# Kernel optimization log

Hardware: AMD Instinct MI355X
Metric: run time of the kernel (lower is better)

## Reference

```python
import jax, jax.numpy as jnp
import numpy as np

P, N, GRID, C, S, STEPS, N_ADJ = 128, 512, 112, 64, 128, 3, 4
HW = GRID * GRID
IN_DIM = C + 2


def _ring_adjacency():
    # prepare_gcn_component builds a ring graph: each vertex connected to
    # n_adj nearest neighbors along the polygon, row-normalized.
    offs = np.concatenate([np.arange(1, N_ADJ // 2 + 1), -np.arange(1, N_ADJ // 2 + 1)])
    A = np.zeros((N, N), np.float32)
    idx = np.arange(N)
    for o in offs:
        A[idx, (idx + o) % N] = 1.0
    A /= A.sum(1, keepdims=True)
    return jnp.asarray(A)


def setup_inputs() -> dict:
    key = jax.random.key(0)
    ks = jax.random.split(key, 10)
    std = 0.01  # matches m.weight.data.normal_(0.0, 0.01)
    return {
        "feature": jax.random.normal(ks[0], (P, HW, C), jnp.float32),
        "init_polys": jax.random.uniform(ks[1], (P, N, 2), jnp.float32),
        "adj": _ring_adjacency(),
        "W1s": jax.random.normal(ks[2], (STEPS, IN_DIM, S), jnp.float32) * std,
        "W1n": jax.random.normal(ks[3], (STEPS, IN_DIM, S), jnp.float32) * std,
        "b1": jnp.zeros((STEPS, S), jnp.float32),
        "W2s": jax.random.normal(ks[4], (STEPS, S, S), jnp.float32) * std,
        "W2n": jax.random.normal(ks[5], (STEPS, S, S), jnp.float32) * std,
        "b2": jnp.zeros((STEPS, S), jnp.float32),
        "Wfc": jax.random.normal(ks[6], (STEPS, S, 2), jnp.float32) * std,
        "bfc": jnp.zeros((STEPS, 2), jnp.float32),
    }


def _gather(feat, ids):
    # feat: [P, HW, C], ids: [P, N] int -> [P, N, C]
    return jnp.take_along_axis(feat, ids[:, :, None], axis=1)


def _nearest_sample(feature, poly):
    # step-0 `sampling` path: gather at floor(coord*grid) flat indices
    X0 = jnp.clip(jnp.floor(poly[..., 0] * GRID), 0, GRID - 1)
    Y0 = jnp.clip(jnp.floor(poly[..., 1] * GRID), 0, GRID - 1)
    ids = (X0 + Y0 * GRID).astype(jnp.int32)
    return _gather(feature, ids)


def _interpolated_sum(feature, poly):
    Xs = poly[..., 0] * GRID
    Ys = poly[..., 1] * GRID
    X0 = jnp.floor(Xs); X1 = X0 + 1.0
    Y0 = jnp.floor(Ys); Y1 = Y0 + 1.0
    w00 = (X1 - Xs) * (Y1 - Ys)
    w01 = (X1 - Xs) * (Ys - Y0)
    w10 = (Xs - X0) * (Y1 - Ys)
    w11 = (Xs - X0) * (Ys - Y0)
    X0c = jnp.clip(X0, 0, GRID - 1).astype(jnp.int32)
    X1c = jnp.clip(X1, 0, GRID - 1).astype(jnp.int32)
    Y0c = jnp.clip(Y0, 0, GRID - 1).astype(jnp.int32)
    Y1c = jnp.clip(Y1, 0, GRID - 1).astype(jnp.int32)
    M00 = _gather(feature, X0c + Y0c * GRID)
    M01 = _gather(feature, X0c + Y1c * GRID)
    M10 = _gather(feature, X1c + Y0c * GRID)
    M11 = _gather(feature, X1c + Y1c * GRID)
    return (w00[..., None] * M00 + w01[..., None] * M01 +
            w10[..., None] * M10 + w11[..., None] * M11)


def _gconv(x, adj, Ws, Wn, b):
    # x: [P, N, D]; adj: [N, N] (shared ring graph)
    nbr = jnp.einsum('nm,pmd->pnd', adj, x)
    return x @ Ws + nbr @ Wn + b


def _gcn(x, adj, i, W1s, W1n, b1, W2s, W2n, b2, Wfc, bfc):
    h = jax.nn.relu(_gconv(x, adj, W1s[i], W1n[i], b1[i]))
    h = jax.nn.relu(_gconv(h, adj, W2s[i], W2n[i], b2[i]))
    return h @ Wfc[i] + bfc[i]  # [P, N, 2]


def reference(feature, init_polys, adj, W1s, W1n, b1, W2s, W2n, b2, Wfc, bfc):
    poly = init_polys
    for i in range(STEPS):
        cnn_feat = _nearest_sample(feature, poly) if i == 0 else _interpolated_sum(feature, poly)
        inp = jnp.concatenate([cnn_feat, poly], axis=2)  # [P, N, C+2]
        pred = _gcn(inp, adj, i, W1s, W1n, b1, W2s, W2n, b2, Wfc, bfc)
        poly = poly + pred
    return poly
```

## Files before the change

### kernel.cpp

```cpp
#include <hip/hip_runtime.h>

#define P_      128
#define NV      512
#define GRID_   112
#define HW_     (GRID_*GRID_)
#define C_      64
#define S_      128

typedef short bf16x8 __attribute__((ext_vector_type(8)));
typedef float f32x4  __attribute__((ext_vector_type(4)));

__device__ __forceinline__ unsigned short f2bf(float x) {
    union { float f; unsigned int u; } v; v.f = x;
    unsigned int r = (v.u + 0x7FFFu + ((v.u >> 16) & 1u)) >> 16;
    return (unsigned short)r;
}
__device__ __forceinline__ float2 up2(unsigned int u) {
    union { unsigned int u; float f; } a, b;
    a.u = u << 16; b.u = u & 0xFFFF0000u;
    return make_float2(a.f, b.f);
}
__device__ __forceinline__ unsigned int pk2(float lo, float hi) {
    return (unsigned int)f2bf(lo) | ((unsigned int)f2bf(hi) << 16);
}

__global__ __launch_bounds__(256) void wprep_kernel(
    const float* __restrict__ W1s, const float* __restrict__ W1n,
    const float* __restrict__ W2s, const float* __restrict__ W2n,
    unsigned short* __restrict__ W1p, unsigned short* __restrict__ W2p)
{
    int idx = blockIdx.x * 256 + threadIdx.x;
    const int N1 = 3 * 5 * 8 * 64 * 8;
    const int N2 = 3 * 8 * 8 * 64 * 8;
    if (idx < N1) {
        int j = idx & 7, lane = (idx >> 3) & 63, nt = (idx >> 9) & 7;
        int ks = (idx >> 12) % 5, step = idx / 20480;
        int n = nt * 16 + (lane & 15);
        int k = ks * 32 + (lane >> 4) * 8 + j;
        float v = 0.f;
        if (k < 66)       v = W1s[(step * 66 + k) * 128 + n];
        else if (k < 132) v = W1n[(step * 66 + (k - 66)) * 128 + n];
        W1p[idx] = f2bf(v);
    } else if (idx < N1 + N2) {
        int e = idx - N1;
        int j = e & 7, lane = (e >> 3) & 63, nt = (e >> 9) & 7;
        int ks = (e >> 12) & 7, step = e >> 15;
        int n = nt * 16 + (lane & 15);
        int k = ks * 32 + (lane >> 4) * 8 + j;
        float v = (k < 128) ? W2s[(step * 128 + k) * 128 + n]
                            : W2n[(step * 128 + (k - 128)) * 128 + n];
        W2p[e] = f2bf(v);
    }
}

__global__ __launch_bounds__(256, 4) void gcn_kernel(
    const float* __restrict__ feature,
    const unsigned short* __restrict__ W1p,
    const float* __restrict__ b1,
    const unsigned short* __restrict__ W2p,
    const float* __restrict__ b2,
    const float* __restrict__ Wfc, const float* __restrict__ bfc,
    const float* __restrict__ poly_in, float* __restrict__ poly_out,
    int nearest)
{
    __shared__ __align__(16) char smem[38016];
    unsigned short* rawS  = (unsigned short*)smem;
    unsigned int*   raw_u = (unsigned int*)smem;
    unsigned int*   A1_u  = (unsigned int*)(smem + 10368);
    unsigned short* h1s   = (unsigned short*)smem;
    unsigned int*   R2_u  = (unsigned int*)(smem + 21120);
    float*          h2    = (float*)smem;
    float2*         polyS = (float2*)(smem + 36864);

    int p = blockIdx.x >> 3, n0 = (blockIdx.x & 7) * 64;
    int wv = threadIdx.x >> 6, lane = threadIdx.x & 63;
    int m = lane & 15, q = lane >> 4;
    int nt0 = wv * 2;

    const float* fb    = feature + (size_t)p * HW_ * C_;
    const float* pbase = poly_in + (size_t)p * NV * 2;

    if (threadIdx.x < 72) {
        int vtx = (n0 + (int)threadIdx.x - 4) & (NV - 1);
        polyS[threadIdx.x] = ((const float2*)pbase)[vtx];
    }
    __syncthreads();

    #pragma unroll 6
    for (int i = 0; i < 18; i++) {
        int u = i * 256 + threadIdx.x;
        int r = u >> 6, ch = u & 63;
        float2 pp = polyS[r];
        float val;
        if (nearest) {
            float X0 = fminf(fmaxf(floorf(pp.x * (float)GRID_), 0.f), (float)(GRID_ - 1));
            float Y0 = fminf(fmaxf(floorf(pp.y * (float)GRID_), 0.f), (float)(GRID_ - 1));
            int id = (int)X0 + (int)Y0 * GRID_;
            val = fb[(size_t)id * C_ + ch];
        } else {
            float Xs = pp.x * (float)GRID_, Ys = pp.y * (float)GRID_;
            float X0 = floorf(Xs), Y0 = floorf(Ys);
            float X1 = X0 + 1.f, Y1 = Y0 + 1.f;
            float ax = X1 - Xs, bx = Xs - X0;
            float ay = Y1 - Ys, by = Ys - Y0;
            int X0c = (int)fminf(fmaxf(X0, 0.f), (float)(GRID_ - 1));
            int X1c = (int)fminf(fmaxf(X1, 0.f), (float)(GRID_ - 1));
            int Y0c = (int)fminf(fmaxf(Y0, 0.f), (float)(GRID_ - 1));
            int Y1c = (int)fminf(fmaxf(Y1, 0.f), (float)(GRID_ - 1));
            float m00 = fb[(size_t)(X0c + Y0c * GRID_) * C_ + ch];
            float m01 = fb[(size_t)(X0c + Y1c * GRID_) * C_ + ch];
            float m10 = fb[(size_t)(X1c + Y0c * GRID_) * C_ + ch];
            float m11 = fb[(size_t)(X1c + Y1c * GRID_) * C_ + ch];
            val = (ax * ay) * m00 + (ax * by) * m01 + (bx * ay) * m10 + (bx * by) * m11;
        }
        rawS[r * 72 + ch] = f2bf(val);
    }
    if (threadIdx.x < 72) {
        float2 pp = polyS[threadIdx.x];
        unsigned short* row = rawS + threadIdx.x * 72;
        row[64] = f2bf(pp.x);
        row[65] = f2bf(pp.y);
        ((unsigned int*)row)[33] = 0u;
        ((unsigned int*)row)[34] = 0u;
        ((unsigned int*)row)[35] = 0u;
    }
    __syncthreads();

    for (int idx = threadIdx.x; idx < 80 * 84; idx += 256) {
        int a = idx / 84, u = idx - a * 84;
        unsigned int val = 0u;
        if (a < 68) {
            if (u < 33) {
                val = raw_u[(a + 2) * 36 + u];
            } else if (u < 66) {
                int uu = u - 33;
                float2 fa = up2(raw_u[a * 36 + uu]),       fb2 = up2(raw_u[(a + 1) * 36 + uu]);
                float2 fc = up2(raw_u[(a + 3) * 36 + uu]), fd  = up2(raw_u[(a + 4) * 36 + uu]);
                val = pk2(0.25f * (fa.x + fb2.x + fc.x + fd.x),
                          0.25f * (fa.y + fb2.y + fc.y + fd.y));
            }
        }
        A1_u[idx] = val;
    }
    __syncthreads();

    f32x4 acc1[5][2];
    #pragma unroll
    for (int i = 0; i < 5; i++) {
        acc1[i][0] = (f32x4){0.f, 0.f, 0.f, 0.f};
        acc1[i][1] = (f32x4){0.f, 0.f, 0.f, 0.f};
    }
    const bf16x8* B1 = (const bf16x8*)W1p;
    const unsigned short* A1s = (const unsigned short*)A1_u;
    #pragma unroll
    for (int ks = 0; ks < 5; ks++) {
        bf16x8 bfr0 = B1[(ks * 8 + nt0) * 64 + lane];
        bf16x8 bfr1 = B1[(ks * 8 + nt0 + 1) * 64 + lane];
        #pragma unroll
        for (int mt = 0; mt < 5; mt++) {
            bf16x8 a = *(const bf16x8*)(A1s + (mt * 16 + m) * 168 + ks * 32 + q * 8);
            acc1[mt][0] = __builtin_amdgcn_mfma_f32_16x16x32_bf16(a, bfr0, acc1[mt][0], 0, 0, 0);
            acc1[mt][1] = __builtin_amdgcn_mfma_f32_16x16x32_bf16(a, bfr1, acc1[mt][1], 0, 0, 0);
        }
    }
    __syncthreads();

    #pragma unroll
    for (int mt = 0; mt < 5; mt++) {
        #pragma unroll
        for (int j = 0; j < 2; j++) {
            int col = (nt0 + j) * 16 + m;
            float bias = b1[col];
            #pragma unroll
            for (int rg = 0; rg < 4; rg++) {
                int row = mt * 16 + q * 4 + rg;
                h1s[row * 132 + col] = f2bf(fmaxf(acc1[mt][j][rg] + bias, 0.f));
            }
        }
    }
    __syncthreads();

    const unsigned int* h1u = (const unsigned int*)h1s;
    for (int idx = threadIdx.x; idx < 64 * 64; idx += 256) {
        int a = idx >> 6, u = idx & 63;
        float2 fa = up2(h1u[a * 66 + u]),       fb2 = up2(h1u[(a + 1) * 66 + u]);
        float2 fc = up2(h1u[(a + 3) * 66 + u]), fd  = up2(h1u[(a + 4) * 66 + u]);
        R2_u[a * 66 + u] = pk2(0.25f * (fa.x + fb2.x + fc.x + fd.x),
                               0.25f * (fa.y + fb2.y + fc.y + fd.y));
    }
    __syncthreads();

    f32x4 acc2[4][2];
    #pragma unroll
    for (int i = 0; i < 4; i++) {
        acc2[i][0] = (f32x4){0.f, 0.f, 0.f, 0.f};
        acc2[i][1] = (f32x4){0.f, 0.f, 0.f, 0.f};
    }
    const bf16x8* B2 = (const bf16x8*)W2p;
    const unsigned short* selfS = h1s + 2 * 132;
    const unsigned short* ringS = (const unsigned short*)R2_u;
    #pragma unroll
    for (int ks = 0; ks < 8; ks++) {
        bf16x8 bfr0 = B2[(ks * 8 + nt0) * 64 + lane];
        bf16x8 bfr1 = B2[(ks * 8 + nt0 + 1) * 64 + lane];
        #pragma unroll
        for (int mt = 0; mt < 4; mt++) {
            const unsigned short* ap = (ks < 4)
                ? selfS + (mt * 16 + m) * 132 + ks * 32 + q * 8
                : ringS + (mt * 16 + m) * 132 + (ks - 4) * 32 + q * 8;
            bf16x8 a = *(const bf16x8*)ap;
            acc2[mt][0] = __builtin_amdgcn_mfma_f32_16x16x32_bf16(a, bfr0, acc2[mt][0], 0, 0, 0);
            acc2[mt][1] = __builtin_amdgcn_mfma_f32_16x16x32_bf16(a, bfr1, acc2[mt][1], 0, 0, 0);
        }
    }
    __syncthreads();

    #pragma unroll
    for (int mt = 0; mt < 4; mt++) {
        #pragma unroll
        for (int j = 0; j < 2; j++) {
            int col = (nt0 + j) * 16 + m;
            float bias = b2[col];
            #pragma unroll
            for (int rg = 0; rg < 4; rg++) {
                int row = mt * 16 + q * 4 + rg;
                h2[row * 129 + col] = fmaxf(acc2[mt][j][rg] + bias, 0.f);
            }
        }
    }
    __syncthreads();

    {
        int t = threadIdx.x;
        int oi = t >> 1, half = t & 1;
        int v = oi >> 1, j = oi & 1;
        const float* hv = h2 + v * 129 + half * 64;
        const float* wf = Wfc + half * 128 + j;
        float s0 = 0.f, s1 = 0.f, s2 = 0.f, s3 = 0.f;
        #pragma unroll
        for (int cc = 0; cc < 64; cc += 4) {
            s0 += hv[cc]     * wf[2 * cc];
            s1 += hv[cc + 1] * wf[2 * cc + 2];
            s2 += hv[cc + 2] * wf[2 * cc + 4];
            s3 += hv[cc + 3] * wf[2 * cc + 6];
        }
        float pr = (s0 + s1) + (s2 + s3) + (half ? 0.f : bfc[j]);
        pr += __shfl_xor(pr, 1);
        if (half == 0) {
            size_t o = ((size_t)p * NV + n0 + v) * 2 + j;
            poly_out[o] = poly_in[o] + pr;
        }
    }
}

extern "C" void kernel_launch(void* const* d_in, const int* in_sizes, int n_in,
                              void* d_out, int out_size, void* d_ws, size_t ws_size,
                              hipStream_t stream)
{
    const float* feature    = (const float*)d_in[0];
    const float* init_polys = (const float*)d_in[1];
    const float* W1s = (const float*)d_in[3];
    const float* W1n = (const float*)d_in[4];
    const float* b1  = (const float*)d_in[5];
    const float* W2s = (const float*)d_in[6];
    const float* W2n = (const float*)d_in[7];
    const float* b2  = (const float*)d_in[8];
    const float* Wfc = (const float*)d_in[9];
    const float* bfc = (const float*)d_in[10];
    float* out = (float*)d_out;

    char* wsb = (char*)d_ws;
    float* polyA = (float*)wsb;                  wsb += (size_t)P_ * NV * 2 * 4;
    float* polyB = (float*)wsb;                  wsb += (size_t)P_ * NV * 2 * 4;
    unsigned short* W1p = (unsigned short*)wsb;  wsb += (size_t)61440 * 2;
    unsigned short* W2p = (unsigned short*)wsb;

    wprep_kernel<<<624, 256, 0, stream>>>(W1s, W1n, W2s, W2n, W1p, W2p);

    const float* pin = init_polys;
    for (int i = 0; i < 3; i++) {
        float* pout = (i == 2) ? out : ((i == 0) ? polyA : polyB);
        gcn_kernel<<<P_ * 8, 256, 0, stream>>>(
            feature,
            W1p + (size_t)i * 20480, b1 + i * 128,
            W2p + (size_t)i * 32768, b2 + i * 128,
            Wfc + i * 256, bfc + i * 2,
            pin, pout, i == 0);
        pin = pout;
    }
}
```

Before: 600.9 us.

## Fuse three GCN step launches into one persistent kernel with grid barriers

Replaces the three per-step kernel launches with a single persistent kernel of 512 blocks, each handling two tiles per step. Steps are separated by a software grid barrier built on an atomic counter and spin-wait. The aim is to remove the launch gaps and tail effects between steps. In exchange each block processes its tiles serially, and correctness depends on all 512 blocks being co-resident, otherwise the barrier can deadlock. It also adds a memset before the launch.

```diff
diff --git a/kernel.cpp b/kernel.cpp
--- a/kernel.cpp
+++ b/kernel.cpp
@@ -53,15 +53,31 @@
     }
 }
 
-__global__ __launch_bounds__(256, 4) void gcn_kernel(
+__device__ __forceinline__ void grid_barrier(unsigned int* ctr, unsigned int target)
+{
+    __syncthreads();
+    if (threadIdx.x == 0) {
+        __threadfence();
+        atomicAdd(ctr, 1u);
+        while (__hip_atomic_load(ctr, __ATOMIC_ACQUIRE,
+                                 __HIP_MEMORY_SCOPE_AGENT) < target) {
+            __builtin_amdgcn_s_sleep(8);
+        }
+    }
+    __syncthreads();
+    __threadfence();
+}
+
+__global__ __launch_bounds__(256, 4) void gcn3_kernel(
     const float* __restrict__ feature,
+    const float* __restrict__ init_polys,
     const unsigned short* __restrict__ W1p,
-    const float* __restrict__ b1,
     const unsigned short* __restrict__ W2p,
-    const float* __restrict__ b2,
+    const float* __restrict__ b1,  const float* __restrict__ b2,
     const float* __restrict__ Wfc, const float* __restrict__ bfc,
-    const float* __restrict__ poly_in, float* __restrict__ poly_out,
-    int nearest)
+    float* __restrict__ polyA, float* __restrict__ polyB,
+    float* __restrict__ out,
+    unsigned int* __restrict__ bar)
 {
     __shared__ __align__(16) char smem[38016];
     unsigned short* rawS  = (unsigned short*)smem;
@@ -72,184 +88,197 @@
     float*          h2    = (float*)smem;
     float2*         polyS = (float2*)(smem + 36864);
 
-    int p = blockIdx.x >> 3, n0 = (blockIdx.x & 7) * 64;
     int wv = threadIdx.x >> 6, lane = threadIdx.x & 63;
     int m = lane & 15, q = lane >> 4;
     int nt0 = wv * 2;
 
-    const float* fb    = feature + (size_t)p * HW_ * C_;
-    const float* pbase = poly_in + (size_t)p * NV * 2;
-
-    if (threadIdx.x < 72) {
-        int vtx = (n0 + (int)threadIdx.x - 4) & (NV - 1);
-        polyS[threadIdx.x] = ((const float2*)pbase)[vtx];
-    }
-    __syncthreads();
-
-    #pragma unroll 6
-    for (int i = 0; i < 18; i++) {
-        int u = i * 256 + threadIdx.x;
-        int r = u >> 6, ch = u & 63;
-        float2 pp = polyS[r];
-        float val;
-        if (nearest) {
-            float X0 = fminf(fmaxf(floorf(pp.x * (float)GRID_), 0.f), (float)(GRID_ - 1));
-            float Y0 = fminf(fmaxf(floorf(pp.y * (float)GRID_), 0.f), (float)(GRID_ - 1));
-            int id = (int)X0 + (int)Y0 * GRID_;
-            val = fb[(size_t)id * C_ + ch];
-        } else {
-            float Xs = pp.x * (float)GRID_, Ys = pp.y * (float)GRID_;
-            float X0 = floorf(Xs), Y0 = floorf(Ys);
-            float X1 = X0 + 1.f, Y1 = Y0 + 1.f;
-            float ax = X1 - Xs, bx = Xs - X0;
-            float ay = Y1 - Ys, by = Ys - Y0;
-            int X0c = (int)fminf(fmaxf(X0, 0.f), (float)(GRID_ - 1));
-            int X1c = (int)fminf(fmaxf(X1, 0.f), (float)(GRID_ - 1));
-            int Y0c = (int)fminf(fmaxf(Y0, 0.f), (float)(GRID_ - 1));
-            int Y1c = (int)fminf(fmaxf(Y1, 0.f), (float)(GRID_ - 1));
-            float m00 = fb[(size_t)(X0c + Y0c * GRID_) * C_ + ch];
-            float m01 = fb[(size_t)(X0c + Y1c * GRID_) * C_ + ch];
-            float m10 = fb[(size_t)(X1c + Y0c * GRID_) * C_ + ch];
-            float m11 = fb[(size_t)(X1c + Y1c * GRID_) * C_ + ch];
-            val = (ax * ay) * m00 + (ax * by) * m01 + (bx * ay) * m10 + (bx * by) * m11;
+    for (int i = 0; i < 3; i++) {
+        const float* poly_in = (i == 0) ? init_polys : ((i == 1) ? polyA : polyB);
+        float* poly_out      = (i == 2) ? out : ((i == 0) ? polyA : polyB);
+        const bf16x8* B1 = (const bf16x8*)(W1p + (size_t)i * 20480);
+        const bf16x8* B2 = (const bf16x8*)(W2p + (size_t)i * 32768);
+        const float* b1i = b1 + i * 128, * b2i = b2 + i * 128;
+        const float* Wfci = Wfc + i * 256, * bfci = bfc + i * 2;
+        int nearest = (i == 0);
+
+        for (int tt = 0; tt < 2; tt++) {
+            int tile = blockIdx.x * 2 + tt;
+            int p = tile >> 3, n0 = (tile & 7) * 64;
+            const float* fb    = feature + (size_t)p * HW_ * C_;
+            const float* pbase = poly_in + (size_t)p * NV * 2;
+
+            if (threadIdx.x < 72) {
+                int vtx = (n0 + (int)threadIdx.x - 4) & (NV - 1);
+                polyS[threadIdx.x] = ((const float2*)pbase)[vtx];
+            }
+            __syncthreads();
+
+            #pragma unroll 6
+            for (int it = 0; it < 18; it++) {
+                int u = it * 256 + threadIdx.x;
+                int r = u >> 6, ch = u & 63;
+                float2 pp = polyS[r];
+                float val;
+                if (nearest) {
+                    float X0 = fminf(fmaxf(floorf(pp.x * (float)GRID_), 0.f), (float)(GRID_ - 1));
+                    float Y0 = fminf(fmaxf(floorf(pp.y * (float)GRID_), 0.f), (float)(GRID_ - 1));
+                    int id = (int)X0 + (int)Y0 * GRID_;
+                    val = fb[(size_t)id * C_ + ch];
+                } else {
+                    float Xs = pp.x * (float)GRID_, Ys = pp.y * (float)GRID_;
+                    float X0 = floorf(Xs), Y0 = floorf(Ys);
+                    float X1 = X0 + 1.f, Y1 = Y0 + 1.f;
+                    float ax = X1 - Xs, bx = Xs - X0;
+                    float ay = Y1 - Ys, by = Ys - Y0;
+                    int X0c = (int)fminf(fmaxf(X0, 0.f), (float)(GRID_ - 1));
+                    int X1c = (int)fminf(fmaxf(X1, 0.f), (float)(GRID_ - 1));
+                    int Y0c = (int)fminf(fmaxf(Y0, 0.f), (float)(GRID_ - 1));
+                    int Y1c = (int)fminf(fmaxf(Y1, 0.f), (float)(GRID_ - 1));
+                    float m00 = fb[(size_t)(X0c + Y0c * GRID_) * C_ + ch];
+                    float m01 = fb[(size_t)(X0c + Y1c * GRID_) * C_ + ch];
+                    float m10 = fb[(size_t)(X1c + Y0c * GRID_) * C_ + ch];
+                    float m11 = fb[(size_t)(X1c + Y1c * GRID_) * C_ + ch];
+                    val = (ax * ay) * m00 + (ax * by) * m01 + (bx * ay) * m10 + (bx * by) * m11;
+                }
+                rawS[r * 72 + ch] = f2bf(val);
+            }
+            if (threadIdx.x < 72) {
+                float2 pp = polyS[threadIdx.x];
+                unsigned short* row = rawS + threadIdx.x * 72;
+                row[64] = f2bf(pp.x);
+                row[65] = f2bf(pp.y);
+                ((unsigned int*)row)[33] = 0u;
+                ((unsigned int*)row)[34] = 0u;
+                ((unsigned int*)row)[35] = 0u;
+            }
+            __syncthreads();
+
+            for (int idx = threadIdx.x; idx < 80 * 84; idx += 256) {
+                int a = idx / 84, u = idx - a * 84;
+                unsigned int val = 0u;
+                if (a < 68) {
+                    if (u < 33) {
+                        val = raw_u[(a + 2) * 36 + u];
+                    } else if (u < 66) {
+                        int uu = u - 33;
+                        float2 fa = up2(raw_u[a * 36 + uu]),       fb2 = up2(raw_u[(a + 1) * 36 + uu]);
+                        float2 fc = up2(raw_u[(a + 3) * 36 + uu]), fd  = up2(raw_u[(a + 4) * 36 + uu]);
+                        val = pk2(0.25f * (fa.x + fb2.x + fc.x + fd.x),
+                                  0.25f * (fa.y + fb2.y + fc.y + fd.y));
+                    }
+                }
+                A1_u[idx] = val;
+            }
+            __syncthreads();
+
+            f32x4 acc1[5][2];
+            #pragma unroll
+            for (int t = 0; t < 5; t++) {
+                acc1[t][0] = (f32x4){0.f, 0.f, 0.f, 0.f};
+                acc1[t][1] = (f32x4){0.f, 0.f, 0.f, 0.f};
+            }
+            const unsigned short* A1s = (const unsigned short*)A1_u;
+            #pragma unroll
+            for (int ks = 0; ks < 5; ks++) {
+                bf16x8 bfr0 = B1[(ks * 8 + nt0) * 64 + lane];
+                bf16x8 bfr1 = B1[(ks * 8 + nt0 + 1) * 64 + lane];
+                #pragma unroll
+                for (int mt = 0; mt < 5; mt++) {
+                    bf16x8 a = *(const bf16x8*)(A1s + (mt * 16 + m) * 168 + ks * 32 + q * 8);
+                    acc1[mt][0] = __builtin_amdgcn_mfma_f32_16x16x32_bf16(a, bfr0, acc1[mt][0], 0, 0, 0);
+                    acc1[mt][1] = __builtin_amdgcn_mfma_f32_16x16x32_bf16(a, bfr1, acc1[mt][1], 0, 0, 0);
+                }
+            }
+            __syncthreads();
+
+            #pragma unroll
+            for (int mt = 0; mt < 5; mt++) {
+                #pragma unroll
+                for (int j = 0; j < 2; j++) {
+                    int col = (nt0 + j) * 16 + m;
+                    float bias = b1i[col];
+                    #pragma unroll
+                    for (int rg = 0; rg < 4; rg++) {
+                        int row = mt * 16 + q * 4 + rg;
+                        h1s[row * 132 + col] = f2bf(fmaxf(acc1[mt][j][rg] + bias, 0.f));
+                    }
+                }
+            }
+            __syncthreads();
+
+            const unsigned int* h1u = (const unsigned int*)h1s;
+            for (int idx = threadIdx.x; idx < 64 * 64; idx += 256) {
+                int a = idx >> 6, u = idx & 63;
+                float2 fa = up2(h1u[a * 66 + u]),       fb2 = up2(h1u[(a + 1) * 66 + u]);
+                float2 fc = up2(h1u[(a + 3) * 66 + u]), fd  = up2(h1u[(a + 4) * 66 + u]);
+                R2_u[a * 66 + u] = pk2(0.25f * (fa.x + fb2.x + fc.x + fd.x),
+                                       0.25f * (fa.y + fb2.y + fc.y + fd.y));
+            }
+            __syncthreads();
+
+            f32x4 acc2[4][2];
+            #pragma unroll
+            for (int t = 0; t < 4; t++) {
+                acc2[t][0] = (f32x4){0.f, 0.f, 0.f, 0.f};
+                acc2[t][1] = (f32x4){0.f, 0.f, 0.f, 0.f};
+            }
+            const unsigned short* selfS = h1s + 2 * 132;
+            const unsigned short* ringS = (const unsigned short*)R2_u;
+            #pragma unroll
+            for (int ks = 0; ks < 8; ks++) {
+                bf16x8 bfr0 = B2[(ks * 8 + nt0) * 64 + lane];
+                bf16x8 bfr1 = B2[(ks * 8 + nt0 + 1) * 64 + lane];
+                #pragma unroll
+                for (int mt = 0; mt < 4; mt++) {
+                    const unsigned short* ap = (ks < 4)
+                        ? selfS + (mt * 16 + m) * 132 + ks * 32 + q * 8
+                        : ringS + (mt * 16 + m) * 132 + (ks - 4) * 32 + q * 8;
+                    bf16x8 a = *(const bf16x8*)ap;
+                    acc2[mt][0] = __builtin_amdgcn_mfma_f32_16x16x32_bf16(a, bfr0, acc2[mt][0], 0, 0, 0);
+                    acc2[mt][1] = __builtin_amdgcn_mfma_f32_16x16x32_bf16(a, bfr1, acc2[mt][1], 0, 0, 0);
+                }
+            }
+            __syncthreads();
+
+            #pragma unroll
+            for (int mt = 0; mt < 4; mt++) {
+                #pragma unroll
+                for (int j = 0; j < 2; j++) {
+                    int col = (nt0 + j) * 16 + m;
+                    float bias = b2i[col];
+                    #pragma unroll
+                    for (int rg = 0; rg < 4; rg++) {
+                        int row = mt * 16 + q * 4 + rg;
+                        h2[row * 129 + col] = fmaxf(acc2[mt][j][rg] + bias, 0.f);
+                    }
+                }
+            }
+            __syncthreads();
+
+            {
+                int t = threadIdx.x;
+                int oi = t >> 1, half = t & 1;
+                int v = oi >> 1, j = oi & 1;
+                const float* hv = h2 + v * 129 + half * 64;
+                const float* wf = Wfci + half * 128 + j;
+                float s0 = 0.f, s1 = 0.f, s2 = 0.f, s3 = 0.f;
+                #pragma unroll
+                for (int cc = 0; cc < 64; cc += 4) {
+                    s0 += hv[cc]     * wf[2 * cc];
+                    s1 += hv[cc + 1] * wf[2 * cc + 2];
+                    s2 += hv[cc + 2] * wf[2 * cc + 4];
+                    s3 += hv[cc + 3] * wf[2 * cc + 6];
+                }
+                float pr = (s0 + s1) + (s2 + s3) + (half ? 0.f : bfci[j]);
+                pr += __shfl_xor(pr, 1);
+                if (half == 0) {
+                    size_t o = ((size_t)p * NV + n0 + v) * 2 + j;
+                    poly_out[o] = poly_in[o] + pr;
+                }
+            }
         }
-        rawS[r * 72 + ch] = f2bf(val);
-    }
-    if (threadIdx.x < 72) {
-        float2 pp = polyS[threadIdx.x];
-        unsigned short* row = rawS + threadIdx.x * 72;
-        row[64] = f2bf(pp.x);
-        row[65] = f2bf(pp.y);
-        ((unsigned int*)row)[33] = 0u;
-        ((unsigned int*)row)[34] = 0u;
-        ((unsigned int*)row)[35] = 0u;
-    }
-    __syncthreads();
-
-    for (int idx = threadIdx.x; idx < 80 * 84; idx += 256) {
-        int a = idx / 84, u = idx - a * 84;
-        unsigned int val = 0u;
-        if (a < 68) {
-            if (u < 33) {
-                val = raw_u[(a + 2) * 36 + u];
-            } else if (u < 66) {
-                int uu = u - 33;
-                float2 fa = up2(raw_u[a * 36 + uu]),       fb2 = up2(raw_u[(a + 1) * 36 + uu]);
-                float2 fc = up2(raw_u[(a + 3) * 36 + uu]), fd  = up2(raw_u[(a + 4) * 36 + uu]);
-                val = pk2(0.25f * (fa.x + fb2.x + fc.x + fd.x),
-                          0.25f * (fa.y + fb2.y + fc.y + fd.y));
-            }
-        }
-        A1_u[idx] = val;
-    }
-    __syncthreads();
-
-    f32x4 acc1[5][2];
-    #pragma unroll
-    for (int i = 0; i < 5; i++) {
-        acc1[i][0] = (f32x4){0.f, 0.f, 0.f, 0.f};
-        acc1[i][1] = (f32x4){0.f, 0.f, 0.f, 0.f};
-    }
-    const bf16x8* B1 = (const bf16x8*)W1p;
-    const unsigned short* A1s = (const unsigned short*)A1_u;
-    #pragma unroll
-    for (int ks = 0; ks < 5; ks++) {
-        bf16x8 bfr0 = B1[(ks * 8 + nt0) * 64 + lane];
-        bf16x8 bfr1 = B1[(ks * 8 + nt0 + 1) * 64 + lane];
-        #pragma unroll
-        for (int mt = 0; mt < 5; mt++) {
-            bf16x8 a = *(const bf16x8*)(A1s + (mt * 16 + m) * 168 + ks * 32 + q * 8);
-            acc1[mt][0] = __builtin_amdgcn_mfma_f32_16x16x32_bf16(a, bfr0, acc1[mt][0], 0, 0, 0);
-            acc1[mt][1] = __builtin_amdgcn_mfma_f32_16x16x32_bf16(a, bfr1, acc1[mt][1], 0, 0, 0);
-        }
-    }
-    __syncthreads();
-
-    #pragma unroll
-    for (int mt = 0; mt < 5; mt++) {
-        #pragma unroll
-        for (int j = 0; j < 2; j++) {
-            int col = (nt0 + j) * 16 + m;
-            float bias = b1[col];
-            #pragma unroll
-            for (int rg = 0; rg < 4; rg++) {
-                int row = mt * 16 + q * 4 + rg;
-                h1s[row * 132 + col] = f2bf(fmaxf(acc1[mt][j][rg] + bias, 0.f));
-            }
-        }
-    }
-    __syncthreads();
-
-    const unsigned int* h1u = (const unsigned int*)h1s;
-    for (int idx = threadIdx.x; idx < 64 * 64; idx += 256) {
-        int a = idx >> 6, u = idx & 63;
-        float2 fa = up2(h1u[a * 66 + u]),       fb2 = up2(h1u[(a + 1) * 66 + u]);
-        float2 fc = up2(h1u[(a + 3) * 66 + u]), fd  = up2(h1u[(a + 4) * 66 + u]);
-        R2_u[a * 66 + u] = pk2(0.25f * (fa.x + fb2.x + fc.x + fd.x),
-                               0.25f * (fa.y + fb2.y + fc.y + fd.y));
-    }
-    __syncthreads();
-
-    f32x4 acc2[4][2];
-    #pragma unroll
-    for (int i = 0; i < 4; i++) {
-        acc2[i][0] = (f32x4){0.f, 0.f, 0.f, 0.f};
-        acc2[i][1] = (f32x4){0.f, 0.f, 0.f, 0.f};
-    }
-    const bf16x8* B2 = (const bf16x8*)W2p;
-    const unsigned short* selfS = h1s + 2 * 132;
-    const unsigned short* ringS = (const unsigned short*)R2_u;
-    #pragma unroll
-    for (int ks = 0; ks < 8; ks++) {
-        bf16x8 bfr0 = B2[(ks * 8 + nt0) * 64 + lane];
-        bf16x8 bfr1 = B2[(ks * 8 + nt0 + 1) * 64 + lane];
-        #pragma unroll
-        for (int mt = 0; mt < 4; mt++) {
-            const unsigned short* ap = (ks < 4)
-                ? selfS + (mt * 16 + m) * 132 + ks * 32 + q * 8
-                : ringS + (mt * 16 + m) * 132 + (ks - 4) * 32 + q * 8;
-            bf16x8 a = *(const bf16x8*)ap;
-            acc2[mt][0] = __builtin_amdgcn_mfma_f32_16x16x32_bf16(a, bfr0, acc2[mt][0], 0, 0, 0);
-            acc2[mt][1] = __builtin_amdgcn_mfma_f32_16x16x32_bf16(a, bfr1, acc2[mt][1], 0, 0, 0);
-        }
-    }
-    __syncthreads();
-
-    #pragma unroll
-    for (int mt = 0; mt < 4; mt++) {
-        #pragma unroll
-        for (int j = 0; j < 2; j++) {
-            int col = (nt0 + j) * 16 + m;
-            float bias = b2[col];
-            #pragma unroll
-            for (int rg = 0; rg < 4; rg++) {
-                int row = mt * 16 + q * 4 + rg;
-                h2[row * 129 + col] = fmaxf(acc2[mt][j][rg] + bias, 0.f);
-            }
-        }
-    }
-    __syncthreads();
-
-    {
-        int t = threadIdx.x;
-        int oi = t >> 1, half = t & 1;
-        int v = oi >> 1, j = oi & 1;
-        const float* hv = h2 + v * 129 + half * 64;
-        const float* wf = Wfc + half * 128 + j;
-        float s0 = 0.f, s1 = 0.f, s2 = 0.f, s3 = 0.f;
-        #pragma unroll
-        for (int cc = 0; cc < 64; cc += 4) {
-            s0 += hv[cc]     * wf[2 * cc];
-            s1 += hv[cc + 1] * wf[2 * cc + 2];
-            s2 += hv[cc + 2] * wf[2 * cc + 4];
-            s3 += hv[cc + 3] * wf[2 * cc + 6];
-        }
-        float pr = (s0 + s1) + (s2 + s3) + (half ? 0.f : bfc[j]);
-        pr += __shfl_xor(pr, 1);
-        if (half == 0) {
-            size_t o = ((size_t)p * NV + n0 + v) * 2 + j;
-            poly_out[o] = poly_in[o] + pr;
-        }
+
+        if (i < 2) grid_barrier(bar + i * 32, 512u);
     }
 }
 
@@ -273,19 +302,12 @@
     float* polyA = (float*)wsb;                  wsb += (size_t)P_ * NV * 2 * 4;
     float* polyB = (float*)wsb;                  wsb += (size_t)P_ * NV * 2 * 4;
     unsigned short* W1p = (unsigned short*)wsb;  wsb += (size_t)61440 * 2;
-    unsigned short* W2p = (unsigned short*)wsb;
-
+    unsigned short* W2p = (unsigned short*)wsb;  wsb += (size_t)98304 * 2;
+    unsigned int* bar = (unsigned int*)wsb;
+
+    hipMemsetAsync(bar, 0, 256, stream);
     wprep_kernel<<<624, 256, 0, stream>>>(W1s, W1n, W2s, W2n, W1p, W2p);
-
-    const float* pin = init_polys;
-    for (int i = 0; i < 3; i++) {
-        float* pout = (i == 2) ? out : ((i == 0) ? polyA : polyB);
-        gcn_kernel<<<P_ * 8, 256, 0, stream>>>(
-            feature,
-            W1p + (size_t)i * 20480, b1 + i * 128,
-            W2p + (size_t)i * 32768, b2 + i * 128,
-            Wfc + i * 256, bfc + i * 2,
-            pin, pout, i == 0);
-        pin = pout;
-    }
-}
+    gcn3_kernel<<<512, 256, 0, stream>>>(
+        feature, init_polys, W1p, W2p, b1, b2, Wfc, bfc,
+        polyA, polyB, out, bar);
+}
```

Measured after the change: 1.015 ms. 68.8% more time.
